# Kernel tuning notes

Measured on AMD Instinct MI355X. Metric: run time of the kernel, lower is better.

## Reference

```python
import jax, jax.numpy as jnp
import numpy as np

C = 256          # simi channels (hardcoded in source)
HM = 128         # feature map spatial size (clamps to 127 in source)
OH = 11          # simi_size_h = int(88/8)
OW = 8           # simi_size   = int(66/8)
MARGIN = 0.1


def setup_inputs() -> dict:
    key = jax.random.key(0)
    ks = jax.random.split(key, 6)
    B, Nf, Nm = 8, 4, 2
    simi = jax.random.normal(ks[0], (B, C, HM, HM), jnp.float32)
    hm = jax.random.normal(ks[1], (B, 1, HM, HM), jnp.float32)
    hm_gt = jax.random.uniform(ks[2], (B, 1, HM, HM), jnp.float32) * 0.9
    hm_gt = hm_gt.at[:, :, ::32, ::32].set(1.0)  # sparse positive centers

    def mk_boxes(k, n):
        k1, k2, k3, k4 = jax.random.split(k, 4)
        x0 = jax.random.randint(k1, (B, n), 0, 96)
        y0 = jax.random.randint(k2, (B, n), 0, 96)
        w = jax.random.randint(k3, (B, n), 8, 30)
        h = jax.random.randint(k4, (B, n), 8, 30)
        return jnp.stack([x0, y0, jnp.minimum(x0 + w, 127), jnp.minimum(y0 + h, 127)], -1).astype(jnp.int32)

    bboxf = mk_boxes(ks[3], Nf)
    bboxm = mk_boxes(ks[4], Nm)
    gamma = jnp.ones((C,), jnp.float32)
    beta = jnp.zeros((C,), jnp.float32)
    return dict(simi=simi, hm=hm, hm_gt=hm_gt, bboxf=bboxf, bboxm=bboxm, gamma=gamma, beta=beta)


def _crop_resize(img_all, bidx, box):
    # Faithful to: slice simi_hm[b,:,y0:y1,x0:x1] then F.interpolate(..., [11,8], 'bilinear')
    # (align_corners=False). Implemented as direct bilinear sampling into the full map.
    x0, y0, x1, y1 = box[0], box[1], box[2], box[3]
    h = (y1 - y0).astype(jnp.float32)
    w = (x1 - x0).astype(jnp.float32)
    sy = jnp.clip((jnp.arange(OH, dtype=jnp.float32) + 0.5) * h / OH - 0.5, 0.0, h - 1.0)
    sx = jnp.clip((jnp.arange(OW, dtype=jnp.float32) + 0.5) * w / OW - 0.5, 0.0, w - 1.0)
    ylo = jnp.floor(sy).astype(jnp.int32)
    xlo = jnp.floor(sx).astype(jnp.int32)
    yhi = jnp.minimum(ylo + 1, y1 - y0 - 1)
    xhi = jnp.minimum(xlo + 1, x1 - x0 - 1)
    wy = sy - ylo
    wx = sx - xlo
    img = img_all[bidx]                       # [C, 128, 128]
    ya, yb = y0 + ylo, y0 + yhi
    xa, xb = x0 + xlo, x0 + xhi
    v00 = img[:, ya[:, None], xa[None, :]]    # [C, 11, 8]
    v01 = img[:, ya[:, None], xb[None, :]]
    v10 = img[:, yb[:, None], xa[None, :]]
    v11 = img[:, yb[:, None], xb[None, :]]
    top = (1.0 - wx) * v00 + wx * v01
    bot = (1.0 - wx) * v10 + wx * v11
    out = (1.0 - wy)[:, None] * top + wy[:, None] * bot
    return out.reshape(-1)                    # flatten in C,H,W order like torch.flatten


_crop_all = jax.vmap(_crop_resize, in_axes=(None, 0, 0))


def _focal_loss(pred, gt):
    # CenterNet focal loss
    pos = (gt == 1.0).astype(pred.dtype)
    neg = 1.0 - pos
    neg_w = jnp.power(1.0 - gt, 4)
    pos_loss = jnp.log(pred) * jnp.square(1.0 - pred) * pos
    neg_loss = jnp.log(1.0 - pred) * jnp.square(pred) * neg_w * neg
    num_pos = pos.sum()
    return -(pos_loss.sum() + neg_loss.sum()) / jnp.maximum(num_pos, 1.0)


def _pdist(a, b):
    # torch PairwiseDistance(2): ||a - b + eps||_2, eps=1e-6
    return jnp.sqrt(jnp.sum(jnp.square(a - b + 1e-6), axis=-1))


def reference(simi, hm, hm_gt, bboxf, bboxm, gamma, beta):
    # BatchNorm2d in training mode (fresh module: batch stats, biased var, eps=1e-5)
    mean = simi.mean((0, 2, 3), keepdims=True)
    var = simi.var((0, 2, 3), keepdims=True)
    simi_n = (simi - mean) / jnp.sqrt(var + 1e-5) * gamma[None, :, None, None] + beta[None, :, None, None]

    B, Nf = bboxf.shape[0], bboxf.shape[1]
    Nm = bboxm.shape[1]
    bidx_f = jnp.repeat(jnp.arange(B), Nf)
    bidx_m = jnp.repeat(jnp.arange(B), Nm)
    faces = _crop_all(simi_n, bidx_f, bboxf.reshape(-1, 4))   # [B*Nf, C*OH*OW]
    masks = _crop_all(simi_n, bidx_m, bboxm.reshape(-1, 4))   # [B*Nm, C*OH*OW]

    total_f = faces.shape[0]
    half = total_f // 2
    # with total_m == total_f//2, match_size == total_m and no random re-fill branch fires
    anchor = faces[:half]
    positive = faces[half:total_f]
    negative = masks
    pos_dist = _pdist(anchor, positive)
    neg_dist = _pdist(anchor, negative)
    triplet = jnp.mean(jnp.maximum(MARGIN + pos_dist - neg_dist, 0.0))

    pred_hm = jnp.clip(jax.nn.sigmoid(hm), 1e-4, 1.0 - 1e-4)  # _sigmoid
    hm_loss = _focal_loss(pred_hm, hm_gt)
    return hm_loss + triplet
```

## Files before the change

### kernel.cpp

```cpp
#include <hip/hip_runtime.h>
#include <math.h>

#define CCH 256
#define HMD 128
#define HW (HMD*HMD)
#define NTOT (8*HW)
#define OH 11
#define OW 8
#define NPIX (OH*OW)
#define NPAIR 16

#define CH_SUM 0
#define CH_SQ  1024
#define TRI    2048
#define FOC    18432

#define NTRIPLET 128
#define NFOCAL   128
#define NPLANE2  1024
#define NBLOCKS  (NTRIPLET + NFOCAL + NPLANE2)

__device__ __forceinline__ void block_reduce2_256(float& a, float& b) {
    #pragma unroll
    for (int off = 32; off > 0; off >>= 1) {
        a += __shfl_down(a, off, 64);
        b += __shfl_down(b, off, 64);
    }
    __shared__ float sa[4], sb[4];
    int wid  = threadIdx.x >> 6;
    int lane = threadIdx.x & 63;
    if (lane == 0) { sa[wid] = a; sb[wid] = b; }
    __syncthreads();
    if (threadIdx.x == 0) {
        a = sa[0] + sa[1] + sa[2] + sa[3];
        b = sb[0] + sb[1] + sb[2] + sb[3];
    }
}

__global__ void mega(const float* __restrict__ simi,
                     const float* __restrict__ hm,
                     const float* __restrict__ gt,
                     const int* __restrict__ bboxf,
                     const int* __restrict__ bboxm,
                     float* __restrict__ ws) {
    const int bid = blockIdx.x;
    const int tid = threadIdx.x;

    if (bid < NTRIPLET) {
        int pair  = bid >> 3;
        int slice = bid & 7;

        __shared__ int   sYA[3][OH], sYB[3][OH], sXA[3][OW], sXB[3][OW];
        __shared__ float sWY[3][OH], sWX[3][OW];
        __shared__ int   sBase[3];

        if (tid < 3) {
            const int* bx;
            int bidx;
            if (tid == 0)      { bx = bboxf + pair * 4;        bidx = pair >> 2; }
            else if (tid == 1) { bx = bboxf + (16 + pair) * 4; bidx = 4 + (pair >> 2); }
            else               { bx = bboxm + pair * 4;        bidx = pair >> 1; }
            int x0 = bx[0], y0 = bx[1], x1 = bx[2], y1 = bx[3];
            float h = (float)(y1 - y0), w = (float)(x1 - x0);
            for (int j = 0; j < OH; ++j) {
                float sy = fminf(fmaxf((j + 0.5f) * h / (float)OH - 0.5f, 0.0f), h - 1.0f);
                int ylo = (int)floorf(sy);
                sYA[tid][j] = y0 + ylo;
                sYB[tid][j] = y0 + min(ylo + 1, y1 - y0 - 1);
                sWY[tid][j] = sy - (float)ylo;
            }
            for (int j = 0; j < OW; ++j) {
                float sx = fminf(fmaxf((j + 0.5f) * w / (float)OW - 0.5f, 0.0f), w - 1.0f);
                int xlo = (int)floorf(sx);
                sXA[tid][j] = x0 + xlo;
                sXB[tid][j] = x0 + min(xlo + 1, x1 - x0 - 1);
                sWX[tid][j] = sx - (float)xlo;
            }
            sBase[tid] = bidx * CCH * HW;
        }
        __syncthreads();

        int cl = tid >> 3;
        int lx = tid & 7;
        int c  = slice * 32 + cl;

        const float* imgA = simi + sBase[0] + c * HW;
        const float* imgP = simi + sBase[1] + c * HW;
        const float* imgN = simi + sBase[2] + c * HW;

        float a1p = 0.f, a2p = 0.f, a1n = 0.f, a2n = 0.f;
        float wxA = sWX[0][lx], wxP = sWX[1][lx], wxN = sWX[2][lx];
        int xaA = sXA[0][lx], xbA = sXB[0][lx];
        int xaP = sXA[1][lx], xbP = sXB[1][lx];
        int xaN = sXA[2][lx], xbN = sXB[2][lx];

        #pragma unroll
        for (int y = 0; y < OH; ++y) {
            float wyA = sWY[0][y], wyP = sWY[1][y], wyN = sWY[2][y];
            int yaA = sYA[0][y] * HMD, ybA = sYB[0][y] * HMD;
            int yaP = sYA[1][y] * HMD, ybP = sYB[1][y] * HMD;
            int yaN = sYA[2][y] * HMD, ybN = sYB[2][y] * HMD;

            float vA, vP, vN;
            {
                float v00 = imgA[yaA + xaA], v01 = imgA[yaA + xbA];
                float v10 = imgA[ybA + xaA], v11 = imgA[ybA + xbA];
                float top = (1.0f - wxA) * v00 + wxA * v01;
                float bot = (1.0f - wxA) * v10 + wxA * v11;
                vA = (1.0f - wyA) * top + wyA * bot;
            }
            {
                float v00 = imgP[yaP + xaP], v01 = imgP[yaP + xbP];
                float v10 = imgP[ybP + xaP], v11 = imgP[ybP + xbP];
                float top = (1.0f - wxP) * v00 + wxP * v01;
                float bot = (1.0f - wxP) * v10 + wxP * v11;
                vP = (1.0f - wyP) * top + wyP * bot;
            }
            {
                float v00 = imgN[yaN + xaN], v01 = imgN[yaN + xbN];
                float v10 = imgN[ybN + xaN], v11 = imgN[ybN + xbN];
                float top = (1.0f - wxN) * v00 + wxN * v01;
                float bot = (1.0f - wxN) * v10 + wxN * v11;
                vN = (1.0f - wyN) * top + wyN * bot;
            }
            float dp = vA - vP; a1p += dp; a2p += dp * dp;
            float dn = vA - vN; a1n += dn; a2n += dn * dn;
        }
        #pragma unroll
        for (int off = 4; off > 0; off >>= 1) {
            a1p += __shfl_down(a1p, off, 8);
            a2p += __shfl_down(a2p, off, 8);
            a1n += __shfl_down(a1n, off, 8);
            a2n += __shfl_down(a2n, off, 8);
        }
        if (lx == 0) {
            float* q = ws + TRI + (pair * 256 + c) * 4;
            q[0] = a1p; q[1] = a2p; q[2] = a1n; q[3] = a2n;
        }
    } else if (bid < NTRIPLET + NFOCAL) {
        int fb = bid - NTRIPLET;
        int i = fb * 256 + tid;
        float4 hv = ((const float4*)hm)[i];
        float4 gv = ((const float4*)gt)[i];
        float lsum = 0.f, npos = 0.f;
        #pragma unroll
        for (int j = 0; j < 4; ++j) {
            float x = (&hv.x)[j], g = (&gv.x)[j];
            float pred = 1.0f / (1.0f + expf(-x));
            pred = fminf(fmaxf(pred, 1e-4f), 1.0f - 1e-4f);
            if (g == 1.0f) {
                float om = 1.0f - pred;
                lsum += logf(pred) * om * om;
                npos += 1.0f;
            } else {
                float gg = 1.0f - g;
                float g2 = gg * gg;
                lsum += logf(1.0f - pred) * pred * pred * (g2 * g2);
            }
        }
        block_reduce2_256(lsum, npos);
        if (tid == 0) { ws[FOC + 2 * fb] = lsum; ws[FOC + 2 * fb + 1] = npos; }
    } else {
        int pb = bid - NTRIPLET - NFOCAL;
        const float4* pa = (const float4*)(simi + (size_t)pb * HW);
        const float4* pc = (const float4*)(simi + (size_t)(pb + 1024) * HW);
        float s = 0.f, s2 = 0.f;
        #pragma unroll
        for (int it = 0; it < 16; ++it) {
            float4 va = pa[it * 256 + tid];
            float4 vb = pc[it * 256 + tid];
            s  += va.x + va.y + va.z + va.w;
            s2 += va.x*va.x + va.y*va.y + va.z*va.z + va.w*va.w;
            s  += vb.x + vb.y + vb.z + vb.w;
            s2 += vb.x*vb.x + vb.y*vb.y + vb.z*vb.z + vb.w*vb.w;
        }
        block_reduce2_256(s, s2);
        if (tid == 0) { ws[CH_SUM + pb] = s; ws[CH_SQ + pb] = s2; }
    }
}

__global__ void finalize(const float* __restrict__ ws,
                         const float* __restrict__ gamma,
                         float* __restrict__ out) {
    __shared__ float s_sh[256], tr[NPAIR], fl[2][2];
    int t = threadIdx.x;

    if (t < 256) {
        float su = 0.f, sq = 0.f;
        #pragma unroll
        for (int b = 0; b < 4; ++b) {
            su += ws[CH_SUM + b * 256 + t];
            sq += ws[CH_SQ  + b * 256 + t];
        }
        const float invn = 1.0f / (float)NTOT;
        float mean = su * invn;
        float var  = sq * invn - mean * mean;
        s_sh[t] = gamma[t] / sqrtf(var + 1e-5f);
    }
    __syncthreads();

    int pr = t >> 6, lane = t & 63;
    float pdl = 0.f, ndl = 0.f;
    #pragma unroll
    for (int k = 0; k < 4; ++k) {
        int c = lane + 64 * k;
        float s = s_sh[c];
        const float* q = ws + TRI + (pr * 256 + c) * 4;
        pdl += s * s * q[1] + 2e-6f * s * q[0];
        ndl += s * s * q[3] + 2e-6f * s * q[2];
    }
    #pragma unroll
    for (int off = 32; off > 0; off >>= 1) {
        pdl += __shfl_down(pdl, off, 64);
        ndl += __shfl_down(ndl, off, 64);
    }
    if (lane == 0) {
        const float e2 = 1e-12f * (float)(CCH * NPIX);
        tr[pr] = fmaxf(0.1f + sqrtf(pdl + e2) - sqrtf(ndl + e2), 0.0f);
    }

    float l = 0.f, np = 0.f;
    if (t < 128) { l = ws[FOC + 2 * t]; np = ws[FOC + 2 * t + 1]; }
    if (t < 128) {
        #pragma unroll
        for (int off = 32; off > 0; off >>= 1) {
            l  += __shfl_down(l, off, 64);
            np += __shfl_down(np, off, 64);
        }
        if ((t & 63) == 0) { fl[t >> 6][0] = l; fl[t >> 6][1] = np; }
    }
    __syncthreads();

    if (t == 0) {
        float trip = 0.f;
        #pragma unroll
        for (int p = 0; p < NPAIR; ++p) trip += tr[p];
        trip *= (1.0f / (float)NPAIR);
        float lt  = fl[0][0] + fl[1][0];
        float npt = fl[0][1] + fl[1][1];
        out[0] = -lt / fmaxf(npt, 1.0f) + trip;
    }
}

extern "C" void kernel_launch(void* const* d_in, const int* in_sizes, int n_in,
                              void* d_out, int out_size, void* d_ws, size_t ws_size,
                              hipStream_t stream) {
    const float* simi  = (const float*)d_in[0];
    const float* hm    = (const float*)d_in[1];
    const float* hm_gt = (const float*)d_in[2];
    const int*   bboxf = (const int*)d_in[3];
    const int*   bboxm = (const int*)d_in[4];
    const float* gamma = (const float*)d_in[5];
    float* out = (float*)d_out;
    float* ws  = (float*)d_ws;

    mega<<<NBLOCKS, 256, 0, stream>>>(simi, hm, hm_gt, bboxf, bboxm, ws);
    finalize<<<1, 1024, 0, stream>>>(ws, gamma, out);
}
```

Before: 34.83 us.

## Fuse finalize into main kernel via last-block atomic counter

Removes the separate finalize kernel launch. The last block to finish, found through an atomic counter reset by a memset, performs the final reduction. Partial results are published and read back with atomics so the last block sees them. This trades one kernel launch for a memset node, and adds atomic traffic and a final reduction done by 256 threads instead of 1024.

Result: slower. 51.13 us (+46.8%).

```diff
diff --git a/kernel.cpp b/kernel.cpp
--- a/kernel.cpp
+++ b/kernel.cpp
@@ -14,11 +14,15 @@
 #define CH_SQ  1024
 #define TRI    2048
 #define FOC    18432
+#define CNT    18688
 
 #define NTRIPLET 128
 #define NFOCAL   128
 #define NPLANE2  1024
 #define NBLOCKS  (NTRIPLET + NFOCAL + NPLANE2)
+
+__device__ __forceinline__ void pub(float* p, float v) { atomicExch(p, v); }
+__device__ __forceinline__ float rd(float* p) { return atomicAdd(p, 0.0f); }
 
 __device__ __forceinline__ void block_reduce2_256(float& a, float& b) {
     #pragma unroll
@@ -42,7 +46,9 @@
                      const float* __restrict__ gt,
                      const int* __restrict__ bboxf,
                      const int* __restrict__ bboxm,
-                     float* __restrict__ ws) {
+                     const float* __restrict__ gamma,
+                     float* __restrict__ ws,
+                     float* __restrict__ out) {
     const int bid = blockIdx.x;
     const int tid = threadIdx.x;
 
@@ -135,7 +141,7 @@
         }
         if (lx == 0) {
             float* q = ws + TRI + (pair * 256 + c) * 4;
-            q[0] = a1p; q[1] = a2p; q[2] = a1n; q[3] = a2n;
+            pub(q + 0, a1p); pub(q + 1, a2p); pub(q + 2, a1n); pub(q + 3, a2n);
         }
     } else if (bid < NTRIPLET + NFOCAL) {
         int fb = bid - NTRIPLET;
@@ -159,7 +165,7 @@
             }
         }
         block_reduce2_256(lsum, npos);
-        if (tid == 0) { ws[FOC + 2 * fb] = lsum; ws[FOC + 2 * fb + 1] = npos; }
+        if (tid == 0) { pub(ws + FOC + 2 * fb, lsum); pub(ws + FOC + 2 * fb + 1, npos); }
     } else {
         int pb = bid - NTRIPLET - NFOCAL;
         const float4* pa = (const float4*)(simi + (size_t)pb * HW);
@@ -175,70 +181,64 @@
             s2 += vb.x*vb.x + vb.y*vb.y + vb.z*vb.z + vb.w*vb.w;
         }
         block_reduce2_256(s, s2);
-        if (tid == 0) { ws[CH_SUM + pb] = s; ws[CH_SQ + pb] = s2; }
-    }
-}
-
-__global__ void finalize(const float* __restrict__ ws,
-                         const float* __restrict__ gamma,
-                         float* __restrict__ out) {
-    __shared__ float s_sh[256], tr[NPAIR], fl[2][2];
-    int t = threadIdx.x;
-
-    if (t < 256) {
-        float su = 0.f, sq = 0.f;
-        #pragma unroll
-        for (int b = 0; b < 4; ++b) {
-            su += ws[CH_SUM + b * 256 + t];
-            sq += ws[CH_SQ  + b * 256 + t];
-        }
-        const float invn = 1.0f / (float)NTOT;
-        float mean = su * invn;
-        float var  = sq * invn - mean * mean;
-        s_sh[t] = gamma[t] / sqrtf(var + 1e-5f);
-    }
-    __syncthreads();
-
-    int pr = t >> 6, lane = t & 63;
+        if (tid == 0) { pub(ws + CH_SUM + pb, s); pub(ws + CH_SQ + pb, s2); }
+    }
+
+    __shared__ int sLast;
+    __syncthreads();
+    if (tid == 0) {
+        unsigned int old = atomicAdd((unsigned int*)(ws + CNT), 1u);
+        sLast = (old == (unsigned int)(NBLOCKS - 1)) ? 1 : 0;
+    }
+    __syncthreads();
+    if (!sLast) return;
+
+    __shared__ float s_sh[256], tr[NPAIR];
+    int t = tid;
+
+    float su = 0.f, sq = 0.f;
+    #pragma unroll
+    for (int b = 0; b < 4; ++b) {
+        su += rd(ws + CH_SUM + b * 256 + t);
+        sq += rd(ws + CH_SQ  + b * 256 + t);
+    }
+    const float invn = 1.0f / (float)NTOT;
+    float mean = su * invn;
+    float var  = sq * invn - mean * mean;
+    s_sh[t] = gamma[t] / sqrtf(var + 1e-5f);
+    __syncthreads();
+
+    int pr = t >> 4, cl2 = t & 15;
     float pdl = 0.f, ndl = 0.f;
     #pragma unroll
-    for (int k = 0; k < 4; ++k) {
-        int c = lane + 64 * k;
-        float s = s_sh[c];
-        const float* q = ws + TRI + (pr * 256 + c) * 4;
-        pdl += s * s * q[1] + 2e-6f * s * q[0];
-        ndl += s * s * q[3] + 2e-6f * s * q[2];
-    }
-    #pragma unroll
-    for (int off = 32; off > 0; off >>= 1) {
-        pdl += __shfl_down(pdl, off, 64);
-        ndl += __shfl_down(ndl, off, 64);
-    }
-    if (lane == 0) {
+    for (int k = 0; k < 16; ++k) {
+        int cc = cl2 + 16 * k;
+        float s = s_sh[cc];
+        float* q = ws + TRI + (pr * 256 + cc) * 4;
+        float q0 = rd(q + 0), q1 = rd(q + 1), q2 = rd(q + 2), q3 = rd(q + 3);
+        pdl += s * s * q1 + 2e-6f * s * q0;
+        ndl += s * s * q3 + 2e-6f * s * q2;
+    }
+    #pragma unroll
+    for (int off = 8; off > 0; off >>= 1) {
+        pdl += __shfl_down(pdl, off, 16);
+        ndl += __shfl_down(ndl, off, 16);
+    }
+    if (cl2 == 0) {
         const float e2 = 1e-12f * (float)(CCH * NPIX);
         tr[pr] = fmaxf(0.1f + sqrtf(pdl + e2) - sqrtf(ndl + e2), 0.0f);
     }
 
     float l = 0.f, np = 0.f;
-    if (t < 128) { l = ws[FOC + 2 * t]; np = ws[FOC + 2 * t + 1]; }
-    if (t < 128) {
-        #pragma unroll
-        for (int off = 32; off > 0; off >>= 1) {
-            l  += __shfl_down(l, off, 64);
-            np += __shfl_down(np, off, 64);
-        }
-        if ((t & 63) == 0) { fl[t >> 6][0] = l; fl[t >> 6][1] = np; }
-    }
-    __syncthreads();
+    if (t < 128) { l = rd(ws + FOC + 2 * t); np = rd(ws + FOC + 2 * t + 1); }
+    block_reduce2_256(l, np);
 
     if (t == 0) {
         float trip = 0.f;
         #pragma unroll
         for (int p = 0; p < NPAIR; ++p) trip += tr[p];
         trip *= (1.0f / (float)NPAIR);
-        float lt  = fl[0][0] + fl[1][0];
-        float npt = fl[0][1] + fl[1][1];
-        out[0] = -lt / fmaxf(npt, 1.0f) + trip;
+        out[0] = -l / fmaxf(np, 1.0f) + trip;
     }
 }
 
@@ -254,6 +254,6 @@
     float* out = (float*)d_out;
     float* ws  = (float*)d_ws;
 
-    mega<<<NBLOCKS, 256, 0, stream>>>(simi, hm, hm_gt, bboxf, bboxm, ws);
-    finalize<<<1, 1024, 0, stream>>>(ws, gamma, out);
+    hipMemsetAsync((unsigned int*)(ws + CNT), 0, sizeof(unsigned int), stream);
+    mega<<<NBLOCKS, 256, 0, stream>>>(simi, hm, hm_gt, bboxf, bboxm, gamma, ws, out);
 }
```
